# Optimization experiments

Hardware: AMD Instinct MI355X
Metric: run time of the kernel (lower is better)

The kernel has to match this reference:

```python
import jax, jax.numpy as jnp
import numpy as np
import math

B, S, L, K, NSTEPS = 32, 128, 4096, 129, 10
PAD = K // 2  # torch: int(kernel.shape[-1]/2)


def _grouped_xcorr(x, w):
    # torch F.conv1d semantics (cross-correlation), groups = channels
    # x: [B,C,L] f32, w: [C,1,K] f32 -> [B,C,L]
    return jax.lax.conv_general_dilated(
        x, w, window_strides=(1,), padding=[(PAD, PAD)],
        dimension_numbers=('NCH', 'OIH', 'NCH'), feature_group_count=x.shape[1])


def _matched_filter(x_re, x_im, k_re, k_im):
    # complex grouped conv with conj(kernel) repeated per pulse
    wc_re = jnp.tile(k_re[None, None, :], (S, 1, 1))
    wc_im = jnp.tile(-k_im[None, None, :], (S, 1, 1))  # conj
    out_re = _grouped_xcorr(x_re, wc_re) - _grouped_xcorr(x_im, wc_im)
    out_im = _grouped_xcorr(x_re, wc_im) + _grouped_xcorr(x_im, wc_re)
    return out_re + 1j * out_im  # complex64 [B,S,L]


def _produce_rd(x, w_mag, w_phase):
    phase = jnp.arctan(w_phase)                    # [B,S]
    norm_mag = S * jax.nn.softmax(w_mag, axis=-1)  # [B,S]
    iq = (norm_mag * jnp.exp(-1j * phase))[..., None] * x
    return jnp.fft.fftshift(jnp.fft.fft(iq, axis=-2), axes=-2)


def _circular_weighted_mean(w):
    # circular weighted mean of index over last axis; returns (magnitude, index)
    N = w.shape[-1]
    ang = (2.0 * jnp.pi / N) * jnp.arange(N, dtype=w.dtype)
    z = jnp.sum(w * jnp.exp(1j * ang), axis=-1)
    return jnp.abs(z), jnp.angle(z) / (2.0 * jnp.pi) * N


def _snr(rd):
    Bn, nfft, Ln = rd.shape
    e = jnp.abs(rd) ** 2                                   # [B,S,L]
    flat_idx = jnp.argmax(e.reshape(Bn, -1), axis=1)
    max_range = flat_idx % Ln                              # [B] (indices: constant wrt grad)
    col = jnp.take_along_axis(e, max_range[:, None, None], axis=2)[..., 0]  # [B,S]
    _, peak_idx = _circular_weighted_mean(col)
    # torch rounds + casts to int -> detached index
    idx = jax.lax.stop_gradient(jnp.round(peak_idx)).astype(jnp.int32) % nfft
    peak = jnp.take_along_axis(col, idx[:, None], axis=1)[:, 0]
    noise = (jnp.sum(col, axis=-1) - peak) / (nfft - 1)
    return 10.0 * jnp.log10(peak) - 10.0 * jnp.log10(noise)


def setup_inputs() -> dict:
    key = jax.random.key(0)
    ks = jax.random.split(key, 5)
    return {
        'x_re': jax.random.normal(ks[0], (B, S, L), jnp.float32),
        'x_im': jax.random.normal(ks[1], (B, S, L), jnp.float32),
        'kernel_re': jax.random.normal(ks[2], (K,), jnp.float32),
        'kernel_im': jax.random.normal(ks[3], (K,), jnp.float32),
        'log_step_mag': -2.0 * jnp.ones((S, NSTEPS), jnp.float32),
        'log_step_phase': -2.0 * jnp.ones((S, NSTEPS), jnp.float32),
        'w_phase_init': jax.random.uniform(ks[4], (B, S), jnp.float32),
    }


def reference(x_re, x_im, kernel_re, kernel_im, log_step_mag, log_step_phase, w_phase_init):
    x = _matched_filter(x_re, x_im, kernel_re, kernel_im)  # [B,S,L] complex64
    w_mag = jnp.ones((B, S), jnp.float32)
    w_phase = w_phase_init

    def loss_sum(wm, wp):
        return jnp.sum(_snr(_produce_rd(x, wm, wp)))

    grad_fn = jax.grad(loss_sum, argnums=(0, 1))
    ln10 = math.log(10.0)
    for i in range(NSTEPS):
        # torch detaches w_mag/w_phase before the inner autograd.grad
        g_mag, g_phase = grad_fn(jax.lax.stop_gradient(w_mag),
                                 jax.lax.stop_gradient(w_phase))
        lr_mag = jnp.exp(log_step_mag[:, i] * ln10)    # 10**log_step
        lr_phase = jnp.exp(log_step_phase[:, i] * ln10)
        w_mag = w_mag + lr_mag * g_mag
        w_phase = w_phase + lr_phase * g_phase
    return jnp.mean(_snr(_produce_rd(x, w_mag, w_phase)))
```

## Files before the change

kernel.cpp:

```cpp
#include <hip/hip_runtime.h>

#define BB 32
#define SS 128
#define LL 4096
#define KK 129
#define NST 10

constexpr double PI_D = 3.141592653589793238462643383279502884;
constexpr double red_sin(double x){
  double x2 = x*x, t = x, r = x;
  t *= -x2/6.0;   r += t;
  t *= -x2/20.0;  r += t;
  t *= -x2/42.0;  r += t;
  t *= -x2/72.0;  r += t;
  t *= -x2/110.0; r += t;
  t *= -x2/156.0; r += t;
  t *= -x2/210.0; r += t;
  t *= -x2/272.0; r += t;
  return r;
}
constexpr double csin_d(double x){
  while (x >  PI_D) x -= 2.0*PI_D;
  while (x < -PI_D) x += 2.0*PI_D;
  if (x >  PI_D*0.5)      x =  PI_D - x;
  else if (x < -PI_D*0.5) x = -PI_D - x;
  return red_sin(x);
}
constexpr double ccos_d(double x){ return csin_d(x + PI_D*0.5); }
struct TWT { float c[64]; float s[64]; };
constexpr TWT make_tw(){
  TWT t{};
  for (int j = 0; j < 64; j++){
    double a = -2.0*PI_D*(double)j/128.0;
    t.c[j] = (float)ccos_d(a);
    t.s[j] = (float)csin_d(a);
  }
  return t;
}
constexpr TWT TW = make_tw();

#define PHYS8(i) ((i) + ((i) >> 3))

__global__ __launch_bounds__(256) void mf_kernel(const float* __restrict__ xr,
                                                 const float* __restrict__ xi,
                                                 const float* __restrict__ kr,
                                                 const float* __restrict__ ki,
                                                 float2* __restrict__ out)
{
  const int row = blockIdx.x >> 1;
  const int l0  = (blockIdx.x & 1) * 2048;
  const int t   = threadIdx.x;
  __shared__ float2 xs[2456];
  __shared__ float2 ks[132];
  if (t < KK) ks[t] = make_float2(kr[t], ki[t]);

  const float* xrr = xr + (size_t)row*LL;
  const float* xir = xi + (size_t)row*LL;
  for (int i4 = t; i4 < 544; i4 += 256){
    const int g0 = l0 - 64 + i4*4;
    float4 a, c;
    if (g0 >= 0 && g0 + 3 < LL){
      a = *(const float4*)(xrr + g0);
      c = *(const float4*)(xir + g0);
    } else {
      float av[4], cv[4];
      #pragma unroll
      for (int e = 0; e < 4; ++e){
        const int g = g0 + e;
        const bool ok = (g >= 0 && g < LL);
        av[e] = ok ? xrr[g] : 0.0f;
        cv[e] = ok ? xir[g] : 0.0f;
      }
      a = make_float4(av[0],av[1],av[2],av[3]);
      c = make_float4(cv[0],cv[1],cv[2],cv[3]);
    }
    const int i = i4*4;
    const int p = PHYS8(i);
    xs[p]   = make_float2(a.x, c.x);
    xs[p+1] = make_float2(a.y, c.y);
    xs[p+2] = make_float2(a.z, c.z);
    xs[p+3] = make_float2(a.w, c.w);
  }
  __syncthreads();

  const int base_l = t*8;
  float wr_[16], wi_[16];
  #pragma unroll
  for (int v = 0; v < 12; v += 2){
    const float4 p = *(const float4*)(&xs[PHYS8(base_l + v)]);
    wr_[v]   = p.x; wi_[v]   = p.y;
    wr_[v+1] = p.z; wi_[v+1] = p.w;
  }

  float2 acc[8];
  #pragma unroll
  for (int j = 0; j < 8; j++) acc[j] = make_float2(0.0f, 0.0f);

  #pragma unroll 1
  for (int q8 = 0; q8 < 8; ++q8){
    #pragma unroll
    for (int qq = 0; qq < 4; ++qq){
      const int q = q8*4 + qq;
      float4 p0, p1;
      const bool doref = (q < 31);
      if (doref){
        const int v0 = base_l + q*4 + 12;
        p0 = *(const float4*)(&xs[PHYS8(v0)]);
        p1 = *(const float4*)(&xs[PHYS8(v0 + 2)]);
      }
      float2 wv[4];
      #pragma unroll
      for (int kk = 0; kk < 4; ++kk) wv[kk] = ks[q*4 + kk];
      #pragma unroll
      for (int kk = 0; kk < 4; ++kk){
        const float wx = wv[kk].x, wy = wv[kk].y;
        #pragma unroll
        for (int j = 0; j < 8; ++j){
          const int sl = (qq*4 + kk + j) & 15;
          const float xvr = wr_[sl], xvi = wi_[sl];
          acc[j].x = fmaf(xvr, wx, acc[j].x);
          acc[j].x = fmaf(xvi, wy, acc[j].x);
          acc[j].y = fmaf(xvi, wx, acc[j].y);
          acc[j].y = fmaf(-xvr, wy, acc[j].y);
        }
      }
      if (doref){
        const int s0 = (qq*4 + 12) & 15;
        wr_[s0]   = p0.x; wi_[s0]   = p0.y;
        wr_[s0+1] = p0.z; wi_[s0+1] = p0.w;
        wr_[s0+2] = p1.x; wi_[s0+2] = p1.y;
        wr_[s0+3] = p1.z; wi_[s0+3] = p1.w;
      }
    }
  }
  {
    const float2 w = ks[128];
    #pragma unroll
    for (int j = 0; j < 8; ++j){
      const float xvr = wr_[j], xvi = wi_[j];
      acc[j].x = fmaf(xvr, w.x, acc[j].x);
      acc[j].x = fmaf(xvi, w.y, acc[j].x);
      acc[j].y = fmaf(xvi, w.x, acc[j].y);
      acc[j].y = fmaf(-xvr, w.y, acc[j].y);
    }
  }

  float4* orow = (float4*)(out + (size_t)row*LL + l0 + base_l);
  #pragma unroll
  for (int q = 0; q < 4; ++q){
    orow[q] = make_float4(acc[2*q].x, acc[2*q].y, acc[2*q+1].x, acc[2*q+1].y);
  }
}

__global__ void init_kernel(const float* __restrict__ wpi,
                            float* __restrict__ w_mag, float* __restrict__ w_phase,
                            float2* __restrict__ cvec, unsigned long long* __restrict__ slots,
                            float* __restrict__ out)
{
  const int i = blockIdx.x*256 + threadIdx.x;
  if (i < BB*SS){
    float wp = wpi[i];
    w_mag[i] = 1.0f;
    w_phase[i] = wp;
    float phi = atanf(wp);
    float s, c;
    sincosf(phi, &s, &c);
    cvec[i] = make_float2(c, -s);
  }
  if (i < BB) slots[i] = 0ull;
  if (i == 0) out[0] = 0.0f;
}

template<int SPAN, int N>
__device__ __forceinline__ void fstage(float2* v){
  #pragma unroll
  for (int b0 = 0; b0 < N; b0 += 2*SPAN){
    #pragma unroll
    for (int j = 0; j < SPAN; j++){
      const int i0 = b0 + j, i1 = b0 + j + SPAN;
      float ax = v[i0].x, ay = v[i0].y, bx = v[i1].x, by = v[i1].y;
      float sx = ax - bx, sy = ay - by;
      v[i0].x = ax + bx; v[i0].y = ay + by;
      const int tj = j * (64 / SPAN);
      if (tj == 0){
        v[i1].x = sx; v[i1].y = sy;
      } else if (tj == 32){
        v[i1].x = sy; v[i1].y = -sx;
      } else {
        const float wr = TW.c[tj], wi = TW.s[tj];
        v[i1].x = sx*wr - sy*wi;
        v[i1].y = sy*wr + sx*wi;
      }
    }
  }
}

__global__ __launch_bounds__(512, 4) void scan_kernel(const float2* __restrict__ xmf,
                                                      const float2* __restrict__ cvec,
                                                      unsigned long long* __restrict__ slots)
{
  const int b = blockIdx.y;
  const int tid = threadIdx.x;
  const int l0 = blockIdx.x * 128;
  __shared__ float2 csh[SS];
  __shared__ float2 xsh[64][130];
  __shared__ unsigned long long wred[8];
  if (tid < SS) csh[tid] = cvec[b*SS + tid];

  const int f = tid >> 2, r = tid & 3;
  float2 v[32];

  #pragma unroll 1
  for (int h = 0; h < 2; ++h){
    __syncthreads();
    const float2* src = xmf + ((size_t)(b*SS + h*64))*LL + l0;
    #pragma unroll
    for (int it = 0; it < 8; ++it){
      const int flat = it*512 + tid;
      const int s1 = flat >> 6;
      const int c4 = flat & 63;
      const float4 vv = *(const float4*)(src + (size_t)s1*LL + c4*2);
      *(float4*)(&xsh[s1][c4*2]) = vv;
    }
    __syncthreads();
    if ((r >> 1) == h){
      #pragma unroll
      for (int j = 0; j < 32; ++j){
        const int rowi = (r & 1)*32 + j;
        const float2 x = xsh[rowi][f];
        const float2 c = csh[r*32 + j];
        v[j].x = c.x*x.x - c.y*x.y;
        v[j].y = c.x*x.y + c.y*x.x;
      }
    }
  }

  {
    const bool hi = (r & 2) != 0;
    const float sgn = hi ? -1.0f : 1.0f;
    const bool odd = (r & 1) != 0;
    #pragma unroll
    for (int j = 0; j < 32; ++j){
      float px = __shfl_xor(v[j].x, 2);
      float py = __shfl_xor(v[j].y, 2);
      float ux = fmaf(sgn, v[j].x, px);
      float uy = fmaf(sgn, v[j].y, py);
      float wr = hi ? (odd ? TW.s[j] : TW.c[j]) : 1.0f;
      float wi = hi ? (odd ? -TW.c[j] : TW.s[j]) : 0.0f;
      v[j].x = ux*wr - uy*wi;
      v[j].y = uy*wr + ux*wi;
    }
  }
  {
    const bool hi = (r & 1) != 0;
    const float sgn = hi ? -1.0f : 1.0f;
    #pragma unroll
    for (int j = 0; j < 32; ++j){
      float px = __shfl_xor(v[j].x, 1);
      float py = __shfl_xor(v[j].y, 1);
      float ux = fmaf(sgn, v[j].x, px);
      float uy = fmaf(sgn, v[j].y, py);
      float wr = hi ? TW.c[2*j] : 1.0f;
      float wi = hi ? TW.s[2*j] : 0.0f;
      v[j].x = ux*wr - uy*wi;
      v[j].y = uy*wr + ux*wi;
    }
  }
  fstage<16,32>(v); fstage<8,32>(v); fstage<4,32>(v); fstage<2,32>(v); fstage<1,32>(v);

  float mm = 0.0f;
  #pragma unroll
  for (int j = 0; j < 32; ++j) mm = fmaxf(mm, v[j].x*v[j].x + v[j].y*v[j].y);
  mm = fmaxf(mm, __shfl_xor(mm, 1));
  mm = fmaxf(mm, __shfl_xor(mm, 2));

  unsigned long long pk = ((unsigned long long)__float_as_uint(mm) << 32) | (unsigned int)(l0 + f);
  #pragma unroll
  for (int m = 4; m < 64; m <<= 1){
    unsigned long long o = __shfl_xor(pk, m);
    if (o > pk) pk = o;
  }
  if ((tid & 63) == 0) wred[tid >> 6] = pk;
  __syncthreads();
  if (tid == 0){
    unsigned long long best = wred[0];
    #pragma unroll
    for (int w = 1; w < 8; ++w) if (wred[w] > best) best = wred[w];
    atomicMax(slots + b, best);
  }
}

__device__ __forceinline__ float wredsum(float v){
  #pragma unroll
  for (int m = 1; m < 64; m <<= 1) v += __shfl_xor(v, m);
  return v;
}
__device__ __forceinline__ float wredmax(float v){
  #pragma unroll
  for (int m = 1; m < 64; m <<= 1) v = fmaxf(v, __shfl_xor(v, m));
  return v;
}
__device__ __forceinline__ float bsum256(float v, float* red4, int t){
  v = wredsum(v);
  __syncthreads();
  if ((t & 63) == 0) red4[t >> 6] = v;
  __syncthreads();
  return red4[0] + red4[1] + red4[2] + red4[3];
}
__device__ __forceinline__ float bmax256(float v, float* red4, int t){
  v = wredmax(v);
  __syncthreads();
  if ((t & 63) == 0) red4[t >> 6] = v;
  __syncthreads();
  return fmaxf(fmaxf(red4[0], red4[1]), fmaxf(red4[2], red4[3]));
}

__global__ __launch_bounds__(256) void step_kernel(const float2* __restrict__ xmf,
                                                   float* __restrict__ w_mag,
                                                   float* __restrict__ w_phase,
                                                   float2* __restrict__ cvec,
                                                   unsigned long long* __restrict__ slots,
                                                   const float* __restrict__ lsm,
                                                   const float* __restrict__ lsp,
                                                   int stepi, int isFinal,
                                                   float* __restrict__ out)
{
  const int b = blockIdx.x, t = threadIdx.x;
  const int s = t >> 1, h = t & 1;
  __shared__ float2 ysh[SS];
  __shared__ float twc[SS], tws[SS];
  __shared__ float red4[4];
  __shared__ float speak;
  __shared__ int sidx;

  const int rbin = (int)(slots[b] & 0xffffffffull);
  const float wm0 = w_mag[b*SS + s];
  const float wp0 = w_phase[b*SS + s];
  const float2 xc = xmf[((size_t)(b*SS + s))*LL + rbin];
  float phi = atanf(wp0);
  float sph, cph;
  sincosf(phi, &sph, &cph);
  {
    int id = t & 127;
    float sv, cv;
    sincosf((float)(2.0*PI_D/128.0) * (float)id, &sv, &cv);
    twc[id] = cv; tws[id] = -sv;
  }
  float mx = bmax256(wm0, red4, t);
  float ex = expf(wm0 - mx);
  float sm = bsum256(ex, red4, t) * 0.5f;
  float m = 128.0f * ex / sm;
  float cre = m*cph, cim = -m*sph;
  ysh[s] = make_float2(cre*xc.x - cim*xc.y, cre*xc.y + cim*xc.x);
  __syncthreads();

  const int k = s;
  float Fr = 0.0f, Fi = 0.0f;
  #pragma unroll 8
  for (int q = 0; q < 64; ++q){
    int s2 = h*64 + q;
    int id = (k*s2) & 127;
    float wr = twc[id], wi = tws[id];
    float2 ys = ysh[s2];
    Fr += wr*ys.x - wi*ys.y;
    Fi += wr*ys.y + wi*ys.x;
  }
  Fr += __shfl_xor(Fr, 1);
  Fi += __shfl_xor(Fi, 1);
  const int u = (k + 64) & 127;
  float colu = Fr*Fr + Fi*Fi;

  float total = bsum256(colu, red4, t) * 0.5f;
  float zre = bsum256(colu * twc[u], red4, t) * 0.5f;
  float zim = bsum256(colu * (-tws[u]), red4, t) * 0.5f;
  if (t == 0){
    float ang = atan2f(zim, zre);
    float pidx = ang * (128.0f/(2.0f*(float)PI_D));
    sidx = ((int)rintf(pidx)) & 127;
  }
  __syncthreads();
  const int idx = sidx;
  if (u == idx && h == 0) speak = colu;
  __syncthreads();
  const float peak = speak;
  const float noise = (total - peak) * (1.0f/127.0f);

  if (isFinal){
    if (t == 0) atomicAdd(out, 10.0f*(log10f(peak) - log10f(noise)) * (1.0f/(float)BB));
    return;
  }

  constexpr float C10 = 4.342944819032518f;
  float g = (u == idx) ? (C10/peak) : (-C10/(127.0f*noise));
  __syncthreads();
  ysh[k] = make_float2(2.0f*g*Fr, 2.0f*g*Fi);
  __syncthreads();

  float Tr = 0.0f, Ti = 0.0f;
  #pragma unroll 8
  for (int q = 0; q < 64; ++q){
    int kk = h*64 + q;
    int id = (s*kk) & 127;
    float wr = twc[id], wi = -tws[id];
    float2 G = ysh[kk];
    Tr += wr*G.x - wi*G.y;
    Ti += wr*G.y + wi*G.x;
  }
  Tr += __shfl_xor(Tr, 1);
  Ti += __shfl_xor(Ti, 1);

  float Hr = xc.x*Tr + xc.y*Ti;
  float Hi = xc.x*Ti - xc.y*Tr;
  float dm   = Hr*cph - Hi*sph;
  float dphi = -m*(Hr*sph + Hi*cph);
  float S1 = bsum256(m*dm, red4, t) * 0.5f;
  float gwm = m*(dm - S1*(1.0f/128.0f));
  float gwp = dphi / (1.0f + wp0*wp0);

  constexpr float LN10 = 2.302585092994046f;
  float lrm = expf(lsm[s*NST + stepi] * LN10);
  float lrp = expf(lsp[s*NST + stepi] * LN10);
  float wm1 = wm0 + lrm*gwm;
  float wp1 = wp0 + lrp*gwp;
  if (h == 0){
    w_mag[b*SS + s] = wm1;
    w_phase[b*SS + s] = wp1;
  }

  float mx2 = bmax256(wm1, red4, t);
  float ex2 = expf(wm1 - mx2);
  float sm2 = bsum256(ex2, red4, t) * 0.5f;
  float m2 = 128.0f * ex2 / sm2;
  float phi2 = atanf(wp1);
  float s2v, c2v;
  sincosf(phi2, &s2v, &c2v);
  if (h == 0) cvec[b*SS + s] = make_float2(m2*c2v, -m2*s2v);
  if (t == 0) slots[b] = 0ull;
}

extern "C" void kernel_launch(void* const* d_in, const int* in_sizes, int n_in,
                              void* d_out, int out_size, void* d_ws, size_t ws_size,
                              hipStream_t stream)
{
  const float* x_re = (const float*)d_in[0];
  const float* x_im = (const float*)d_in[1];
  const float* k_re = (const float*)d_in[2];
  const float* k_im = (const float*)d_in[3];
  const float* lsm  = (const float*)d_in[4];
  const float* lsp  = (const float*)d_in[5];
  const float* wpi  = (const float*)d_in[6];
  float* out = (float*)d_out;

  char* ws = (char*)d_ws;
  size_t off = 0;
  float2* xmf = (float2*)(ws + off);                 off += (size_t)BB*SS*LL*sizeof(float2);
  unsigned long long* slots = (unsigned long long*)(ws + off); off += 256;
  float* w_mag   = (float*)(ws + off);               off += (size_t)BB*SS*4;
  float* w_phase = (float*)(ws + off);               off += (size_t)BB*SS*4;
  float2* cvec   = (float2*)(ws + off);              off += (size_t)BB*SS*8;
  if (ws_size < off) return;

  mf_kernel<<<BB*SS*2, 256, 0, stream>>>(x_re, x_im, k_re, k_im, xmf);
  init_kernel<<<(BB*SS + 255)/256, 256, 0, stream>>>(wpi, w_mag, w_phase, cvec, slots, out);
  for (int i = 0; i < NST; i++){
    scan_kernel<<<dim3(LL/128, BB), 512, 0, stream>>>(xmf, cvec, slots);
    step_kernel<<<BB, 256, 0, stream>>>(xmf, w_mag, w_phase, cvec, slots, lsm, lsp, i, 0, out);
  }
  scan_kernel<<<dim3(LL/128, BB), 512, 0, stream>>>(xmf, cvec, slots);
  step_kernel<<<BB, 256, 0, stream>>>(xmf, w_mag, w_phase, cvec, slots, lsm, lsp, 0, 1, out);
}
```

Baseline: 789.1 us.

## Transpose matched-filter output once so scan reads contiguous pulse columns

```diff
diff --git a/kernel.cpp b/kernel.cpp
--- a/kernel.cpp
+++ b/kernel.cpp
@@ -152,6 +152,35 @@
   }
 }
 
+__global__ __launch_bounds__(512) void tr_kernel(const float2* __restrict__ xmf,
+                                                 float2* __restrict__ xt)
+{
+  const int b = blockIdx.y;
+  const int l0 = blockIdx.x * 64;
+  const int tid = threadIdx.x;
+  __shared__ float ldr[64][129];
+  __shared__ float ldi[64][129];
+  #pragma unroll
+  for (int it = 0; it < 8; ++it){
+    const int flat = it*512 + tid;
+    const int s  = flat >> 5;
+    const int c4 = flat & 31;
+    const float4 p = *(const float4*)(xmf + ((size_t)(b*SS + s))*LL + l0 + 2*c4);
+    ldr[2*c4][s]   = p.x;  ldi[2*c4][s]   = p.y;
+    ldr[2*c4+1][s] = p.z;  ldi[2*c4+1][s] = p.w;
+  }
+  __syncthreads();
+  #pragma unroll
+  for (int it = 0; it < 8; ++it){
+    const int flat = it*512 + tid;
+    const int dl = flat >> 6;
+    const int s4 = flat & 63;
+    const float r0 = ldr[dl][2*s4], r1 = ldr[dl][2*s4+1];
+    const float i0 = ldi[dl][2*s4], i1 = ldi[dl][2*s4+1];
+    *(float4*)(xt + ((size_t)b*LL + l0 + dl)*SS + 2*s4) = make_float4(r0, i0, r1, i1);
+  }
+}
+
 __global__ void init_kernel(const float* __restrict__ wpi,
                             float* __restrict__ w_mag, float* __restrict__ w_phase,
                             float2* __restrict__ cvec, unsigned long long* __restrict__ slots,
@@ -195,46 +224,10 @@
   }
 }
 
-__global__ __launch_bounds__(512, 4) void scan_kernel(const float2* __restrict__ xmf,
-                                                      const float2* __restrict__ cvec,
-                                                      unsigned long long* __restrict__ slots)
-{
-  const int b = blockIdx.y;
-  const int tid = threadIdx.x;
-  const int l0 = blockIdx.x * 128;
-  __shared__ float2 csh[SS];
-  __shared__ float2 xsh[64][130];
-  __shared__ unsigned long long wred[8];
-  if (tid < SS) csh[tid] = cvec[b*SS + tid];
-
-  const int f = tid >> 2, r = tid & 3;
-  float2 v[32];
-
-  #pragma unroll 1
-  for (int h = 0; h < 2; ++h){
-    __syncthreads();
-    const float2* src = xmf + ((size_t)(b*SS + h*64))*LL + l0;
-    #pragma unroll
-    for (int it = 0; it < 8; ++it){
-      const int flat = it*512 + tid;
-      const int s1 = flat >> 6;
-      const int c4 = flat & 63;
-      const float4 vv = *(const float4*)(src + (size_t)s1*LL + c4*2);
-      *(float4*)(&xsh[s1][c4*2]) = vv;
-    }
-    __syncthreads();
-    if ((r >> 1) == h){
-      #pragma unroll
-      for (int j = 0; j < 32; ++j){
-        const int rowi = (r & 1)*32 + j;
-        const float2 x = xsh[rowi][f];
-        const float2 c = csh[r*32 + j];
-        v[j].x = c.x*x.x - c.y*x.y;
-        v[j].y = c.x*x.y + c.y*x.x;
-      }
-    }
-  }
-
+__device__ __forceinline__ void scan_fft_tail(float2* v, int r, int tid, int l,
+                                              unsigned long long* wred, int nwave,
+                                              unsigned long long* slot)
+{
   {
     const bool hi = (r & 2) != 0;
     const float sgn = hi ? -1.0f : 1.0f;
@@ -274,7 +267,7 @@
   mm = fmaxf(mm, __shfl_xor(mm, 1));
   mm = fmaxf(mm, __shfl_xor(mm, 2));
 
-  unsigned long long pk = ((unsigned long long)__float_as_uint(mm) << 32) | (unsigned int)(l0 + f);
+  unsigned long long pk = ((unsigned long long)__float_as_uint(mm) << 32) | (unsigned int)l;
   #pragma unroll
   for (int m = 4; m < 64; m <<= 1){
     unsigned long long o = __shfl_xor(pk, m);
@@ -284,10 +277,82 @@
   __syncthreads();
   if (tid == 0){
     unsigned long long best = wred[0];
+    for (int w = 1; w < nwave; ++w) if (wred[w] > best) best = wred[w];
+    atomicMax(slot, best);
+  }
+}
+
+__global__ __launch_bounds__(256) void scan_t_kernel(const float2* __restrict__ xt,
+                                                     const float2* __restrict__ cvec,
+                                                     unsigned long long* __restrict__ slots)
+{
+  const int b = blockIdx.y;
+  const int tid = threadIdx.x;
+  const int f = tid >> 2, r = tid & 3;
+  const int l = blockIdx.x*64 + f;
+  __shared__ float2 csh[SS];
+  __shared__ unsigned long long wred[4];
+  if (tid < SS) csh[tid] = cvec[b*SS + tid];
+  __syncthreads();
+
+  const float2* col = xt + ((size_t)b*LL + l)*SS + r*32;
+  float2 v[32];
+  #pragma unroll
+  for (int i = 0; i < 8; ++i){
+    const float4 p = ((const float4*)col)[i];
+    v[2*i]   = make_float2(p.x, p.y);
+    v[2*i+1] = make_float2(p.z, p.w);
+  }
+  #pragma unroll
+  for (int j = 0; j < 32; ++j){
+    const float2 c = csh[r*32 + j];
+    const float2 x = v[j];
+    v[j].x = c.x*x.x - c.y*x.y;
+    v[j].y = c.x*x.y + c.y*x.x;
+  }
+  scan_fft_tail(v, r, tid, l, wred, 4, slots + b);
+}
+
+__global__ __launch_bounds__(512, 4) void scan_o_kernel(const float2* __restrict__ xmf,
+                                                        const float2* __restrict__ cvec,
+                                                        unsigned long long* __restrict__ slots)
+{
+  const int b = blockIdx.y;
+  const int tid = threadIdx.x;
+  const int l0 = blockIdx.x * 128;
+  __shared__ float2 csh[SS];
+  __shared__ float2 xsh[64][130];
+  __shared__ unsigned long long wred[8];
+  if (tid < SS) csh[tid] = cvec[b*SS + tid];
+
+  const int f = tid >> 2, r = tid & 3;
+  float2 v[32];
+
+  #pragma unroll 1
+  for (int h = 0; h < 2; ++h){
+    __syncthreads();
+    const float2* src = xmf + ((size_t)(b*SS + h*64))*LL + l0;
     #pragma unroll
-    for (int w = 1; w < 8; ++w) if (wred[w] > best) best = wred[w];
-    atomicMax(slots + b, best);
-  }
+    for (int it = 0; it < 8; ++it){
+      const int flat = it*512 + tid;
+      const int s1 = flat >> 6;
+      const int c4 = flat & 63;
+      const float4 vv = *(const float4*)(src + (size_t)s1*LL + c4*2);
+      *(float4*)(&xsh[s1][c4*2]) = vv;
+    }
+    __syncthreads();
+    if ((r >> 1) == h){
+      #pragma unroll
+      for (int j = 0; j < 32; ++j){
+        const int rowi = (r & 1)*32 + j;
+        const float2 x = xsh[rowi][f];
+        const float2 c = csh[r*32 + j];
+        v[j].x = c.x*x.x - c.y*x.y;
+        v[j].y = c.x*x.y + c.y*x.x;
+      }
+    }
+  }
+  scan_fft_tail(v, r, tid, l0 + f, wred, 8, slots + b);
 }
 
 __device__ __forceinline__ float wredsum(float v){
@@ -316,6 +381,7 @@
 }
 
 __global__ __launch_bounds__(256) void step_kernel(const float2* __restrict__ xmf,
+                                                   const float2* __restrict__ xt, int useT,
                                                    float* __restrict__ w_mag,
                                                    float* __restrict__ w_phase,
                                                    float2* __restrict__ cvec,
@@ -336,7 +402,8 @@
   const int rbin = (int)(slots[b] & 0xffffffffull);
   const float wm0 = w_mag[b*SS + s];
   const float wp0 = w_phase[b*SS + s];
-  const float2 xc = xmf[((size_t)(b*SS + s))*LL + rbin];
+  const float2 xc = useT ? xt[((size_t)b*LL + rbin)*SS + s]
+                         : xmf[((size_t)(b*SS + s))*LL + rbin];
   float phi = atanf(wp0);
   float sph, cph;
   sincosf(phi, &sph, &cph);
@@ -458,14 +525,21 @@
   float* w_mag   = (float*)(ws + off);               off += (size_t)BB*SS*4;
   float* w_phase = (float*)(ws + off);               off += (size_t)BB*SS*4;
   float2* cvec   = (float2*)(ws + off);              off += (size_t)BB*SS*8;
-  if (ws_size < off) return;
+  const size_t off_base = off;
+  float2* xt = (float2*)(ws + off);                  off += (size_t)BB*SS*LL*sizeof(float2);
+  const int useT = (ws_size >= off) ? 1 : 0;
+  if (ws_size < off_base) return;
 
   mf_kernel<<<BB*SS*2, 256, 0, stream>>>(x_re, x_im, k_re, k_im, xmf);
   init_kernel<<<(BB*SS + 255)/256, 256, 0, stream>>>(wpi, w_mag, w_phase, cvec, slots, out);
+  if (useT) tr_kernel<<<dim3(LL/64, BB), 512, 0, stream>>>(xmf, xt);
+
   for (int i = 0; i < NST; i++){
-    scan_kernel<<<dim3(LL/128, BB), 512, 0, stream>>>(xmf, cvec, slots);
-    step_kernel<<<BB, 256, 0, stream>>>(xmf, w_mag, w_phase, cvec, slots, lsm, lsp, i, 0, out);
-  }
-  scan_kernel<<<dim3(LL/128, BB), 512, 0, stream>>>(xmf, cvec, slots);
-  step_kernel<<<BB, 256, 0, stream>>>(xmf, w_mag, w_phase, cvec, slots, lsm, lsp, 0, 1, out);
-}
+    if (useT) scan_t_kernel<<<dim3(LL/64, BB), 256, 0, stream>>>(xt, cvec, slots);
+    else      scan_o_kernel<<<dim3(LL/128, BB), 512, 0, stream>>>(xmf, cvec, slots);
+    step_kernel<<<BB, 256, 0, stream>>>(xmf, xt, useT, w_mag, w_phase, cvec, slots, lsm, lsp, i, 0, out);
+  }
+  if (useT) scan_t_kernel<<<dim3(LL/64, BB), 256, 0, stream>>>(xt, cvec, slots);
+  else      scan_o_kernel<<<dim3(LL/128, BB), 512, 0, stream>>>(xmf, cvec, slots);
+  step_kernel<<<BB, 256, 0, stream>>>(xmf, xt, useT, w_mag, w_phase, cvec, slots, lsm, lsp, 0, 1, out);
+}
```

Result: slower. 808.9 us (+2.5%).
